# Kernel tuning notes

Hardware: AMD Instinct MI355X
Metric: run time of the kernel (lower is better)

Reference implementation:

```python
import jax, jax.numpy as jnp
import numpy as np

B, N, QDIM, KVDIM, DIM, H = 2, 4096, 256, 256, 256, 8


def setup_inputs() -> dict:
    key = jax.random.key(0)
    ks = jax.random.split(key, 8)
    s = 0.02
    return {
        "x": jax.random.normal(ks[0], (B, N, QDIM), jnp.float32),
        "y": jax.random.normal(ks[1], (B, N, KVDIM), jnp.float32),
        "Wq": jax.random.normal(ks[2], (DIM, QDIM), jnp.float32) * s,
        "bq": jnp.zeros((DIM,), jnp.float32),
        "Wk": jax.random.normal(ks[3], (DIM, KVDIM), jnp.float32) * s,
        "bk": jnp.zeros((DIM,), jnp.float32),
        "Wv": jax.random.normal(ks[4], (DIM, KVDIM), jnp.float32) * s,
        "bv": jnp.zeros((DIM,), jnp.float32),
        "Wo": jax.random.normal(ks[5], (DIM, DIM), jnp.float32) * s,
        "bo": jnp.zeros((DIM,), jnp.float32),
    }


def reference(x, y, Wq, bq, Wk, bk, Wv, bv, Wo, bo):
    b, n, _ = x.shape
    h = H
    scale = KVDIM ** (-0.5)  # note: full kv_dim, as in the source
    q = x @ Wq.T + bq  # (b, n, dim)
    k = y @ Wk.T + bk
    v = y @ Wv.T + bv
    def split(t):
        return t.reshape(b, -1, h, DIM // h).transpose(0, 2, 1, 3)  # b h n d
    q, k, v = split(q), split(k), split(v)
    dots = jnp.einsum('bhid,bhjd->bhij', q, k) * scale
    attn = jax.nn.softmax(dots, axis=-1)
    out = jnp.einsum('bhij,bhjd->bhid', attn, v)
    out = out.transpose(0, 2, 1, 3).reshape(b, n, DIM)  # b n (h d)
    out = out @ Wo.T + bo
    return out
```

## Files before the change

kernel.cpp:

```cpp
#include <hip/hip_runtime.h>

#define BATCH 2
#define SEQ   4096
#define DIM   256
#define NHEAD 8
#define HDIM  32
#define ROWS  (BATCH * SEQ)

typedef __attribute__((ext_vector_type(8))) short short8;
typedef __attribute__((ext_vector_type(8))) unsigned short ushort8;
typedef __attribute__((ext_vector_type(4))) unsigned short ushortx4;
typedef __attribute__((ext_vector_type(4))) float floatx4;
typedef __attribute__((ext_vector_type(2))) unsigned int uintx2;

static __device__ __forceinline__ unsigned short f2bf(float f) {
    union { float f; unsigned u; } v; v.f = f;
    unsigned r = v.u + 0x7fffu + ((v.u >> 16) & 1u);
    return (unsigned short)(r >> 16);
}
static __device__ __forceinline__ unsigned fbits(float f) {
    union { float f; unsigned u; } v; v.f = f; return v.u;
}
static __device__ __forceinline__ unsigned pack2(float a, float b) {
    return __builtin_amdgcn_perm(fbits(b), fbits(a), 0x07060302u);
}

static __device__ __forceinline__ void g2l16(const void* g, void* l) {
    __builtin_amdgcn_global_load_lds(
        (const __attribute__((address_space(1))) unsigned int*)g,
        (__attribute__((address_space(3))) unsigned int*)l, 16, 0, 0);
}

__global__ __launch_bounds__(256, 2) void qkv_kernel(
    const float* __restrict__ x, const float* __restrict__ y,
    const float* __restrict__ Wq, const float* __restrict__ Wk,
    const float* __restrict__ Wv,
    const float* __restrict__ bq, const float* __restrict__ bk, const float* __restrict__ bv,
    unsigned short* __restrict__ qo, unsigned short* __restrict__ ko,
    unsigned short* __restrict__ vto) {
    __shared__ unsigned short Abuf[8][64][32];
    const int tid = threadIdx.x, lane = tid & 63, wave = tid >> 6;
    const int ql = lane & 15, quad = lane >> 4;
    const int mat = blockIdx.y;
    const int m0 = blockIdx.x * 64;
    const float* A = (mat == 0) ? x : y;
    const float* W = (mat == 0) ? Wq : (mat == 1) ? Wk : Wv;
    const float* bias = (mat == 0) ? bq : (mat == 1) ? bk : bv;

    {
        const int row = tid >> 2, c8 = (tid & 3) * 8;
        const int swz = ((tid & 3) ^ ((row >> 1) & 3)) * 8;
        const float* src = A + (long)(m0 + row) * DIM + c8;
#pragma unroll
        for (int kb = 0; kb < 8; kb++) {
            float4 v0 = *(const float4*)(src + kb * 32);
            float4 v1 = *(const float4*)(src + kb * 32 + 4);
            ushort8 o;
            o[0] = f2bf(v0.x); o[1] = f2bf(v0.y); o[2] = f2bf(v0.z); o[3] = f2bf(v0.w);
            o[4] = f2bf(v1.x); o[5] = f2bf(v1.y); o[6] = f2bf(v1.z); o[7] = f2bf(v1.w);
            *(ushort8*)(&Abuf[kb][row][swz]) = o;
        }
    }
    __syncthreads();
    const int n0 = wave * 64;
    const int akey = (quad ^ ((ql >> 1) & 3)) * 8;
    floatx4 acc[4][4] = {};
    for (int kb = 0; kb < 8; kb++) {
        short8 wf[4], af[4];
#pragma unroll
        for (int u = 0; u < 4; u++) {
            const float* wr = W + (long)(n0 + u*16 + ql) * DIM + kb*32 + quad*8;
            float4 a = *(const float4*)wr;
            float4 c = *(const float4*)(wr + 4);
            short8 o;
            o[0] = (short)f2bf(a.x); o[1] = (short)f2bf(a.y); o[2] = (short)f2bf(a.z); o[3] = (short)f2bf(a.w);
            o[4] = (short)f2bf(c.x); o[5] = (short)f2bf(c.y); o[6] = (short)f2bf(c.z); o[7] = (short)f2bf(c.w);
            wf[u] = o;
        }
#pragma unroll
        for (int t = 0; t < 4; t++)
            af[t] = *(const short8*)(&Abuf[kb][t*16 + ql][akey]);
        if (mat < 2) {
#pragma unroll
            for (int t = 0; t < 4; t++)
#pragma unroll
                for (int u = 0; u < 4; u++)
                    acc[t][u] = __builtin_amdgcn_mfma_f32_16x16x32_bf16(wf[u], af[t], acc[t][u], 0, 0, 0);
        } else {
#pragma unroll
            for (int t = 0; t < 4; t++)
#pragma unroll
                for (int u = 0; u < 4; u++)
                    acc[t][u] = __builtin_amdgcn_mfma_f32_16x16x32_bf16(af[t], wf[u], acc[t][u], 0, 0, 0);
        }
    }
    if (mat < 2) {
        const float scale = (mat == 0) ? 0.09016844005556021f : 1.0f;
        unsigned short* out = (mat == 0) ? qo : ko;
#pragma unroll
        for (int t = 0; t < 4; t++) {
            int m = m0 + t*16 + ql;
#pragma unroll
            for (int u = 0; u < 4; u++) {
                int n = n0 + u*16 + quad*4;
                float4 b4 = *(const float4*)(bias + n);
                ushortx4 o;
                o.x = f2bf((acc[t][u][0] + b4.x) * scale);
                o.y = f2bf((acc[t][u][1] + b4.y) * scale);
                o.z = f2bf((acc[t][u][2] + b4.z) * scale);
                o.w = f2bf((acc[t][u][3] + b4.w) * scale);
                *(ushortx4*)(out + (long)m * DIM + n) = o;
            }
        }
    } else {
#pragma unroll
        for (int t = 0; t < 4; t++) {
            int mb = m0 + t*16 + quad*4;
            int bi = mb >> 12, i0 = mb & (SEQ - 1);
#pragma unroll
            for (int u = 0; u < 4; u++) {
                int n = n0 + u*16 + ql;
                float b = bias[n];
                ushortx4 o;
                o.x = f2bf(acc[t][u][0] + b);
                o.y = f2bf(acc[t][u][1] + b);
                o.z = f2bf(acc[t][u][2] + b);
                o.w = f2bf(acc[t][u][3] + b);
                *(ushortx4*)(vto + ((long)(bi * DIM + n)) * SEQ + i0) = o;
            }
        }
    }
}

__global__ __launch_bounds__(256, 2) void attn_kernel(
    const unsigned short* __restrict__ qb, const unsigned short* __restrict__ kbuf,
    const unsigned short* __restrict__ vT, unsigned short* __restrict__ ao) {
    __shared__ unsigned short K0[128 * 32], K1[128 * 32];
    __shared__ unsigned short V0[32 * 128], V1[32 * 128];
    __shared__ unsigned short P[4][32][72];
    const int tid = threadIdx.x, lane = tid & 63, wave = tid >> 6;
    const int ql = lane & 15, quad = lane >> 4;
    const int bh = blockIdx.y, b = bh >> 3, h = bh & 7;
    const int q0 = blockIdx.x * 128 + wave * 32;

    const unsigned short* qrow = qb   + (long)b * SEQ * DIM + h * HDIM;
    const unsigned short* krow = kbuf + (long)b * SEQ * DIM + h * HDIM;
    const unsigned short* vrow = vT   + (long)(b * DIM + h * HDIM) * SEQ;

    short8 qf[2];
#pragma unroll
    for (int t = 0; t < 2; t++)
        qf[t] = *(const short8*)(qrow + (long)(q0 + t*16 + ql) * DIM + quad*8);

    short8 ones;
#pragma unroll
    for (int i = 0; i < 8; i++) ones[i] = (short)0x3F80;

    const int kc0 = wave * 2, kc1 = wave * 2 + 1;
    const int klr = lane >> 2, kswz = ((lane & 3) ^ ((lane >> 3) & 3)) * 8;
    const unsigned short* kg0 = krow + (long)(kc0*16 + klr) * DIM + kswz;
    const unsigned short* kg1 = krow + (long)(kc1*16 + klr) * DIM + kswz;
    const int vlr = lane >> 4, vcl = lane & 15;
    const int vsw0 = (vcl ^ ((kc0*4 + vlr) & 7)) * 8;
    const int vsw1 = (vcl ^ ((kc1*4 + vlr) & 7)) * 8;
    const unsigned short* vg0 = vrow + (long)(kc0*4 + vlr) * SEQ + vsw0;
    const unsigned short* vg1 = vrow + (long)(kc1*4 + vlr) * SEQ + vsw1;

    const int kro = (quad ^ ((ql >> 1) & 3)) * 8;
    const int vmask = ql & 7;

    floatx4 acc[2][2] = {};
    floatx4 accL[2] = {};

    auto stage = [&](unsigned short* Kd, unsigned short* Vd, int kv0) {
        g2l16(kg0 + (long)kv0 * DIM, Kd + kc0 * 512);
        g2l16(kg1 + (long)kv0 * DIM, Kd + kc1 * 512);
        g2l16(vg0 + kv0, Vd + kc0 * 512);
        g2l16(vg1 + kv0, Vd + kc1 * 512);
    };
    auto compute = [&](const unsigned short* Ks, const unsigned short* Vs) {
#pragma unroll
        for (int half = 0; half < 2; ++half) {
#pragma unroll
            for (int mt = 0; mt < 4; ++mt) {
                short8 kf = *(const short8*)(Ks + (half*64 + mt*16 + ql) * 32 + kro);
#pragma unroll
                for (int t = 0; t < 2; t++) {
                    floatx4 z = {};
                    floatx4 s = __builtin_amdgcn_mfma_f32_16x16x32_bf16(kf, qf[t], z, 0, 0, 0);
                    float p0 = __builtin_amdgcn_exp2f(s[0]);
                    float p1 = __builtin_amdgcn_exp2f(s[1]);
                    float p2 = __builtin_amdgcn_exp2f(s[2]);
                    float p3 = __builtin_amdgcn_exp2f(s[3]);
                    uintx2 w;
                    w.x = pack2(p0, p1);
                    w.y = pack2(p2, p3);
                    *(uintx2*)(&P[wave][t*16 + ql][mt*16 + quad*4]) = w;
                }
            }
#pragma unroll
            for (int ks = 0; ks < 2; ++ks) {
                short8 pf[2];
#pragma unroll
                for (int t = 0; t < 2; t++)
                    pf[t] = *(const short8*)(&P[wave][t*16 + ql][ks*32 + quad*8]);
#pragma unroll
                for (int t = 0; t < 2; t++)
                    accL[t] = __builtin_amdgcn_mfma_f32_16x16x32_bf16(ones, pf[t], accL[t], 0, 0, 0);
#pragma unroll
                for (int dt = 0; dt < 2; ++dt) {
                    int vco = ((8*half + 4*ks + quad) ^ vmask) * 8;
                    short8 vf = *(const short8*)(Vs + (dt*16 + ql) * 128 + vco);
#pragma unroll
                    for (int t = 0; t < 2; t++)
                        acc[dt][t] = __builtin_amdgcn_mfma_f32_16x16x32_bf16(vf, pf[t], acc[dt][t], 0, 0, 0);
                }
            }
        }
    };

    stage(K0, V0, 0);
    __syncthreads();
    for (int it = 0; it < SEQ / 128; it += 2) {
        if (it + 1 < SEQ / 128) stage(K1, V1, (it + 1) * 128);
        compute(K0, V0);
        __syncthreads();
        if (it + 2 < SEQ / 128) stage(K0, V0, (it + 2) * 128);
        compute(K1, V1);
        __syncthreads();
    }

    float inv[2];
#pragma unroll
    for (int t = 0; t < 2; t++) inv[t] = 1.0f / accL[t][0];
#pragma unroll
    for (int dt = 0; dt < 2; dt++)
#pragma unroll
        for (int t = 0; t < 2; t++) {
            ushortx4 o;
            o.x = f2bf(acc[dt][t][0] * inv[t]);
            o.y = f2bf(acc[dt][t][1] * inv[t]);
            o.z = f2bf(acc[dt][t][2] * inv[t]);
            o.w = f2bf(acc[dt][t][3] * inv[t]);
            *(ushortx4*)(ao + (long)(b*SEQ + q0 + t*16 + ql) * DIM + h*HDIM + dt*16 + quad*4) = o;
        }
}

__global__ __launch_bounds__(256, 2) void oproj_kernel(
    const unsigned short* __restrict__ A, const float* __restrict__ W,
    const float* __restrict__ bias, float* __restrict__ out) {
    __shared__ unsigned short Abuf[8][32][32];
    const int tid = threadIdx.x, lane = tid & 63, wave = tid >> 6;
    const int ql = lane & 15, quad = lane >> 4;
    const int m0 = blockIdx.x * 32;
    const int swz = ((lane & 3) ^ ((lane >> 3) & 3)) * 8;
#pragma unroll
    for (int j = 0; j < 4; j++) {
        int c = wave * 4 + j;
        int kb = c >> 1, hf = (c & 1) * 16;
        const unsigned short* g = A + (long)(m0 + hf + (lane >> 2)) * DIM + kb*32 + swz;
        g2l16(g, &Abuf[kb][hf][0]);
    }
    __syncthreads();
    const int n0 = wave * 64;
    const int akey = (quad ^ ((ql >> 1) & 3)) * 8;
    floatx4 acc[2][4] = {};
    for (int kb = 0; kb < 8; kb++) {
        short8 wf[4], af[2];
#pragma unroll
        for (int u = 0; u < 4; u++) {
            const float* wr = W + (long)(n0 + u*16 + ql) * DIM + kb*32 + quad*8;
            float4 a = *(const float4*)wr;
            float4 c = *(const float4*)(wr + 4);
            short8 o;
            o[0] = (short)f2bf(a.x); o[1] = (short)f2bf(a.y); o[2] = (short)f2bf(a.z); o[3] = (short)f2bf(a.w);
            o[4] = (short)f2bf(c.x); o[5] = (short)f2bf(c.y); o[6] = (short)f2bf(c.z); o[7] = (short)f2bf(c.w);
            wf[u] = o;
        }
#pragma unroll
        for (int t = 0; t < 2; t++)
            af[t] = *(const short8*)(&Abuf[kb][t*16 + ql][akey]);
#pragma unroll
        for (int t = 0; t < 2; t++)
#pragma unroll
            for (int u = 0; u < 4; u++)
                acc[t][u] = __builtin_amdgcn_mfma_f32_16x16x32_bf16(wf[u], af[t], acc[t][u], 0, 0, 0);
    }
#pragma unroll
    for (int t = 0; t < 2; t++) {
        int m = m0 + t*16 + ql;
#pragma unroll
        for (int u = 0; u < 4; u++) {
            int n = n0 + u*16 + quad*4;
            float4 b4 = *(const float4*)(bias + n);
            float4 o;
            o.x = acc[t][u][0] + b4.x;
            o.y = acc[t][u][1] + b4.y;
            o.z = acc[t][u][2] + b4.z;
            o.w = acc[t][u][3] + b4.w;
            *(float4*)(out + (long)m * DIM + n) = o;
        }
    }
}

extern "C" void kernel_launch(void* const* d_in, const int* in_sizes, int n_in,
                              void* d_out, int out_size, void* d_ws, size_t ws_size,
                              hipStream_t stream) {
    const float* x  = (const float*)d_in[0];
    const float* y  = (const float*)d_in[1];
    const float* Wq = (const float*)d_in[2];
    const float* bq = (const float*)d_in[3];
    const float* Wk = (const float*)d_in[4];
    const float* bk = (const float*)d_in[5];
    const float* Wv = (const float*)d_in[6];
    const float* bv = (const float*)d_in[7];
    const float* Wo = (const float*)d_in[8];
    const float* bo = (const float*)d_in[9];
    float* out = (float*)d_out;

    const long NX = (long)ROWS * DIM;
    unsigned short* qbf  = (unsigned short*)d_ws;
    unsigned short* kbf  = qbf + NX;
    unsigned short* vTb  = kbf + NX;
    unsigned short* attn = vTb + NX;

    qkv_kernel<<<dim3(ROWS / 64, 3), dim3(256), 0, stream>>>(
        x, y, Wq, Wk, Wv, bq, bk, bv, qbf, kbf, vTb);

    attn_kernel<<<dim3(SEQ / 128, BATCH * NHEAD), dim3(256), 0, stream>>>(
        qbf, kbf, vTb, attn);

    oproj_kernel<<<dim3(ROWS / 32), dim3(256), 0, stream>>>(
        attn, Wo, bo, out);
}
```

Measured before the change: 169.9 us.

## Pre-convert inputs to bf16, retile projections, and enlarge attention query tile

Adds a separate conversion kernel that turns x, y and all weight matrices into bf16 once. The projection kernels can then stream A tiles with direct global-to-LDS loads, double-buffered, and read bf16 weights with no per-tile conversion. The QKV and output projections are retiled into 64x128 blocks with a 2x2 wave layout. Attention now handles 64 queries per wave with 64-key chunks and launch bounds of one block per SM. The cost is an extra kernel launch, extra memory traffic through the bf16 staging buffers, and a __syncthreads in every k-step; attention occupancy may also drop.

```diff
diff --git a/kernel.cpp b/kernel.cpp
--- a/kernel.cpp
+++ b/kernel.cpp
@@ -8,7 +8,6 @@
 #define ROWS  (BATCH * SEQ)
 
 typedef __attribute__((ext_vector_type(8))) short short8;
-typedef __attribute__((ext_vector_type(8))) unsigned short ushort8;
 typedef __attribute__((ext_vector_type(4))) unsigned short ushortx4;
 typedef __attribute__((ext_vector_type(4))) float floatx4;
 typedef __attribute__((ext_vector_type(2))) unsigned int uintx2;
@@ -24,85 +23,97 @@
 static __device__ __forceinline__ unsigned pack2(float a, float b) {
     return __builtin_amdgcn_perm(fbits(b), fbits(a), 0x07060302u);
 }
-
 static __device__ __forceinline__ void g2l16(const void* g, void* l) {
     __builtin_amdgcn_global_load_lds(
         (const __attribute__((address_space(1))) unsigned int*)g,
         (__attribute__((address_space(3))) unsigned int*)l, 16, 0, 0);
 }
 
-__global__ __launch_bounds__(256, 2) void qkv_kernel(
+__global__ __launch_bounds__(256) void convert_kernel(
     const float* __restrict__ x, const float* __restrict__ y,
     const float* __restrict__ Wq, const float* __restrict__ Wk,
-    const float* __restrict__ Wv,
+    const float* __restrict__ Wv, const float* __restrict__ Wo,
+    unsigned short* __restrict__ xb, unsigned short* __restrict__ yb,
+    unsigned short* __restrict__ Wqb, unsigned short* __restrict__ Wkb,
+    unsigned short* __restrict__ Wvb, unsigned short* __restrict__ Wob) {
+    const long NX = (long)ROWS * DIM;
+    const long NW = (long)DIM * DIM;
+    long e0 = ((long)blockIdx.x * 256 + threadIdx.x) * 4;
+    const float* src; unsigned short* dst; long off;
+    if      (e0 < NX)          { src = x;  dst = xb;  off = e0; }
+    else if (e0 < 2*NX)        { src = y;  dst = yb;  off = e0 - NX; }
+    else if (e0 < 2*NX + NW)   { src = Wq; dst = Wqb; off = e0 - 2*NX; }
+    else if (e0 < 2*NX + 2*NW) { src = Wk; dst = Wkb; off = e0 - 2*NX - NW; }
+    else if (e0 < 2*NX + 3*NW) { src = Wv; dst = Wvb; off = e0 - 2*NX - 2*NW; }
+    else if (e0 < 2*NX + 4*NW) { src = Wo; dst = Wob; off = e0 - 2*NX - 3*NW; }
+    else return;
+    float4 v = *(const float4*)(src + off);
+    ushortx4 o;
+    o.x = f2bf(v.x); o.y = f2bf(v.y); o.z = f2bf(v.z); o.w = f2bf(v.w);
+    *(ushortx4*)(dst + off) = o;
+}
+
+__global__ __launch_bounds__(256, 2) void qkv_kernel(
+    const unsigned short* __restrict__ xb, const unsigned short* __restrict__ yb,
+    const unsigned short* __restrict__ Wq, const unsigned short* __restrict__ Wk,
+    const unsigned short* __restrict__ Wv,
     const float* __restrict__ bq, const float* __restrict__ bk, const float* __restrict__ bv,
     unsigned short* __restrict__ qo, unsigned short* __restrict__ ko,
     unsigned short* __restrict__ vto) {
-    __shared__ unsigned short Abuf[8][64][32];
+    __shared__ unsigned short Ab0[64 * 32], Ab1[64 * 32];
     const int tid = threadIdx.x, lane = tid & 63, wave = tid >> 6;
     const int ql = lane & 15, quad = lane >> 4;
-    const int mat = blockIdx.y;
+    const int wm = wave & 1, wn = wave >> 1;
+    const int mat = blockIdx.z;
     const int m0 = blockIdx.x * 64;
-    const float* A = (mat == 0) ? x : y;
-    const float* W = (mat == 0) ? Wq : (mat == 1) ? Wk : Wv;
+    const int n0 = blockIdx.y * 128;
+    const unsigned short* A = (mat == 0) ? xb : yb;
+    const unsigned short* W = (mat == 0) ? Wq : (mat == 1) ? Wk : Wv;
     const float* bias = (mat == 0) ? bq : (mat == 1) ? bk : bv;
 
-    {
-        const int row = tid >> 2, c8 = (tid & 3) * 8;
-        const int swz = ((tid & 3) ^ ((row >> 1) & 3)) * 8;
-        const float* src = A + (long)(m0 + row) * DIM + c8;
-#pragma unroll
-        for (int kb = 0; kb < 8; kb++) {
-            float4 v0 = *(const float4*)(src + kb * 32);
-            float4 v1 = *(const float4*)(src + kb * 32 + 4);
-            ushort8 o;
-            o[0] = f2bf(v0.x); o[1] = f2bf(v0.y); o[2] = f2bf(v0.z); o[3] = f2bf(v0.w);
-            o[4] = f2bf(v1.x); o[5] = f2bf(v1.y); o[6] = f2bf(v1.z); o[7] = f2bf(v1.w);
-            *(ushort8*)(&Abuf[kb][row][swz]) = o;
-        }
-    }
+    const unsigned short* ag = A + (long)(m0 + wave*16 + (lane >> 2)) * DIM
+                                 + ((lane & 3) ^ ((lane >> 3) & 3)) * 8;
+    unsigned short* ad0 = Ab0 + wave * 512;
+    unsigned short* ad1 = Ab1 + wave * 512;
+    const int akey = (quad ^ ((ql >> 1) & 3)) * 8;
+
+    floatx4 acc[2][4] = {};
+    g2l16(ag, ad0);
     __syncthreads();
-    const int n0 = wave * 64;
-    const int akey = (quad ^ ((ql >> 1) & 3)) * 8;
-    floatx4 acc[4][4] = {};
     for (int kb = 0; kb < 8; kb++) {
-        short8 wf[4], af[4];
-#pragma unroll
-        for (int u = 0; u < 4; u++) {
-            const float* wr = W + (long)(n0 + u*16 + ql) * DIM + kb*32 + quad*8;
-            float4 a = *(const float4*)wr;
-            float4 c = *(const float4*)(wr + 4);
-            short8 o;
-            o[0] = (short)f2bf(a.x); o[1] = (short)f2bf(a.y); o[2] = (short)f2bf(a.z); o[3] = (short)f2bf(a.w);
-            o[4] = (short)f2bf(c.x); o[5] = (short)f2bf(c.y); o[6] = (short)f2bf(c.z); o[7] = (short)f2bf(c.w);
-            wf[u] = o;
-        }
-#pragma unroll
-        for (int t = 0; t < 4; t++)
-            af[t] = *(const short8*)(&Abuf[kb][t*16 + ql][akey]);
+        if (kb < 7) g2l16(ag + (kb + 1) * 32, (kb & 1) ? ad0 : ad1);
+        const unsigned short* Ას = (kb & 1) ? Ab1 : Ab0;
+        short8 wf[4], af[2];
+#pragma unroll
+        for (int u = 0; u < 4; u++)
+            wf[u] = *(const short8*)(W + (long)(n0 + wn*64 + u*16 + ql) * DIM + kb*32 + quad*8);
+#pragma unroll
+        for (int t = 0; t < 2; t++)
+            af[t] = *(const short8*)(Ას + (wm*32 + t*16 + ql) * 32 + akey);
         if (mat < 2) {
 #pragma unroll
-            for (int t = 0; t < 4; t++)
+            for (int t = 0; t < 2; t++)
 #pragma unroll
                 for (int u = 0; u < 4; u++)
                     acc[t][u] = __builtin_amdgcn_mfma_f32_16x16x32_bf16(wf[u], af[t], acc[t][u], 0, 0, 0);
         } else {
 #pragma unroll
-            for (int t = 0; t < 4; t++)
+            for (int t = 0; t < 2; t++)
 #pragma unroll
                 for (int u = 0; u < 4; u++)
                     acc[t][u] = __builtin_amdgcn_mfma_f32_16x16x32_bf16(af[t], wf[u], acc[t][u], 0, 0, 0);
         }
+        __syncthreads();
     }
     if (mat < 2) {
         const float scale = (mat == 0) ? 0.09016844005556021f : 1.0f;
         unsigned short* out = (mat == 0) ? qo : ko;
 #pragma unroll
-        for (int t = 0; t < 4; t++) {
-            int m = m0 + t*16 + ql;
+        for (int t = 0; t < 2; t++) {
+            int m = m0 + wm*32 + t*16 + ql;
 #pragma unroll
             for (int u = 0; u < 4; u++) {
-                int n = n0 + u*16 + quad*4;
+                int n = n0 + wn*64 + u*16 + quad*4;
                 float4 b4 = *(const float4*)(bias + n);
                 ushortx4 o;
                 o.x = f2bf((acc[t][u][0] + b4.x) * scale);
@@ -114,12 +125,12 @@
         }
     } else {
 #pragma unroll
-        for (int t = 0; t < 4; t++) {
-            int mb = m0 + t*16 + quad*4;
+        for (int t = 0; t < 2; t++) {
+            int mb = m0 + wm*32 + t*16 + quad*4;
             int bi = mb >> 12, i0 = mb & (SEQ - 1);
 #pragma unroll
             for (int u = 0; u < 4; u++) {
-                int n = n0 + u*16 + ql;
+                int n = n0 + wn*64 + u*16 + ql;
                 float b = bias[n];
                 ushortx4 o;
                 o.x = f2bf(acc[t][u][0] + b);
@@ -132,111 +143,103 @@
     }
 }
 
-__global__ __launch_bounds__(256, 2) void attn_kernel(
+__global__ __launch_bounds__(256, 1) void attn_kernel(
     const unsigned short* __restrict__ qb, const unsigned short* __restrict__ kbuf,
     const unsigned short* __restrict__ vT, unsigned short* __restrict__ ao) {
-    __shared__ unsigned short K0[128 * 32], K1[128 * 32];
-    __shared__ unsigned short V0[32 * 128], V1[32 * 128];
-    __shared__ unsigned short P[4][32][72];
+    __shared__ unsigned short K0[64 * 32], K1[64 * 32];
+    __shared__ unsigned short V0[32 * 64], V1[32 * 64];
+    __shared__ unsigned short P[4][64][72];
     const int tid = threadIdx.x, lane = tid & 63, wave = tid >> 6;
     const int ql = lane & 15, quad = lane >> 4;
     const int bh = blockIdx.y, b = bh >> 3, h = bh & 7;
-    const int q0 = blockIdx.x * 128 + wave * 32;
+    const int q0 = blockIdx.x * 256 + wave * 64;
 
     const unsigned short* qrow = qb   + (long)b * SEQ * DIM + h * HDIM;
     const unsigned short* krow = kbuf + (long)b * SEQ * DIM + h * HDIM;
     const unsigned short* vrow = vT   + (long)(b * DIM + h * HDIM) * SEQ;
 
-    short8 qf[2];
-#pragma unroll
-    for (int t = 0; t < 2; t++)
+    short8 qf[4];
+#pragma unroll
+    for (int t = 0; t < 4; t++)
         qf[t] = *(const short8*)(qrow + (long)(q0 + t*16 + ql) * DIM + quad*8);
 
     short8 ones;
 #pragma unroll
     for (int i = 0; i < 8; i++) ones[i] = (short)0x3F80;
 
-    const int kc0 = wave * 2, kc1 = wave * 2 + 1;
-    const int klr = lane >> 2, kswz = ((lane & 3) ^ ((lane >> 3) & 3)) * 8;
-    const unsigned short* kg0 = krow + (long)(kc0*16 + klr) * DIM + kswz;
-    const unsigned short* kg1 = krow + (long)(kc1*16 + klr) * DIM + kswz;
-    const int vlr = lane >> 4, vcl = lane & 15;
-    const int vsw0 = (vcl ^ ((kc0*4 + vlr) & 7)) * 8;
-    const int vsw1 = (vcl ^ ((kc1*4 + vlr) & 7)) * 8;
-    const unsigned short* vg0 = vrow + (long)(kc0*4 + vlr) * SEQ + vsw0;
-    const unsigned short* vg1 = vrow + (long)(kc1*4 + vlr) * SEQ + vsw1;
-
+    const unsigned short* kg = krow + (long)(wave*16 + (lane >> 2)) * DIM
+                                    + ((lane & 3) ^ ((lane >> 3) & 3)) * 8;
+    const unsigned short* vg = vrow + (long)(wave*8 + (lane >> 3)) * SEQ
+                                    + ((lane & 7) ^ (lane >> 3)) * 8;
+    unsigned short* kd0 = K0 + wave * 512;  unsigned short* kd1 = K1 + wave * 512;
+    unsigned short* vd0 = V0 + wave * 512;  unsigned short* vd1 = V1 + wave * 512;
     const int kro = (quad ^ ((ql >> 1) & 3)) * 8;
     const int vmask = ql & 7;
 
-    floatx4 acc[2][2] = {};
-    floatx4 accL[2] = {};
-
-    auto stage = [&](unsigned short* Kd, unsigned short* Vd, int kv0) {
-        g2l16(kg0 + (long)kv0 * DIM, Kd + kc0 * 512);
-        g2l16(kg1 + (long)kv0 * DIM, Kd + kc1 * 512);
-        g2l16(vg0 + kv0, Vd + kc0 * 512);
-        g2l16(vg1 + kv0, Vd + kc1 * 512);
+    floatx4 acc[2][4] = {};
+    floatx4 accL[4] = {};
+
+    auto compute = [&](const unsigned short* Ks, const unsigned short* Vs) {
+#pragma unroll
+        for (int mt = 0; mt < 4; ++mt) {
+            short8 kf = *(const short8*)(Ks + (mt*16 + ql) * 32 + kro);
+#pragma unroll
+            for (int t = 0; t < 4; t++) {
+                floatx4 z = {};
+                floatx4 s = __builtin_amdgcn_mfma_f32_16x16x32_bf16(kf, qf[t], z, 0, 0, 0);
+                float p0 = __builtin_amdgcn_exp2f(s[0]);
+                float p1 = __builtin_amdgcn_exp2f(s[1]);
+                float p2 = __builtin_amdgcn_exp2f(s[2]);
+                float p3 = __builtin_amdgcn_exp2f(s[3]);
+                uintx2 w;
+                w.x = pack2(p0, p1);
+                w.y = pack2(p2, p3);
+                *(uintx2*)(&P[wave][t*16 + ql][mt*16 + quad*4]) = w;
+            }
+        }
+#pragma unroll
+        for (int ks = 0; ks < 2; ++ks) {
+            short8 pf[4];
+#pragma unroll
+            for (int t = 0; t < 4; t++)
+                pf[t] = *(const short8*)(&P[wave][t*16 + ql][ks*32 + quad*8]);
+#pragma unroll
+            for (int t = 0; t < 4; t++)
+                accL[t] = __builtin_amdgcn_mfma_f32_16x16x32_bf16(ones, pf[t], accL[t], 0, 0, 0);
+#pragma unroll
+            for (int dt = 0; dt < 2; ++dt) {
+                short8 vf = *(const short8*)(Vs + (dt*16 + ql) * 64 + ((ks*4 + quad) ^ vmask) * 8);
+#pragma unroll
+                for (int t = 0; t < 4; t++)
+                    acc[dt][t] = __builtin_amdgcn_mfma_f32_16x16x32_bf16(vf, pf[t], acc[dt][t], 0, 0, 0);
+            }
+        }
     };
-    auto compute = [&](const unsigned short* Ks, const unsigned short* Vs) {
-#pragma unroll
-        for (int half = 0; half < 2; ++half) {
-#pragma unroll
-            for (int mt = 0; mt < 4; ++mt) {
-                short8 kf = *(const short8*)(Ks + (half*64 + mt*16 + ql) * 32 + kro);
-#pragma unroll
-                for (int t = 0; t < 2; t++) {
-                    floatx4 z = {};
-                    floatx4 s = __builtin_amdgcn_mfma_f32_16x16x32_bf16(kf, qf[t], z, 0, 0, 0);
-                    float p0 = __builtin_amdgcn_exp2f(s[0]);
-                    float p1 = __builtin_amdgcn_exp2f(s[1]);
-                    float p2 = __builtin_amdgcn_exp2f(s[2]);
-                    float p3 = __builtin_amdgcn_exp2f(s[3]);
-                    uintx2 w;
-                    w.x = pack2(p0, p1);
-                    w.y = pack2(p2, p3);
-                    *(uintx2*)(&P[wave][t*16 + ql][mt*16 + quad*4]) = w;
-                }
-            }
-#pragma unroll
-            for (int ks = 0; ks < 2; ++ks) {
-                short8 pf[2];
-#pragma unroll
-                for (int t = 0; t < 2; t++)
-                    pf[t] = *(const short8*)(&P[wave][t*16 + ql][ks*32 + quad*8]);
-#pragma unroll
-                for (int t = 0; t < 2; t++)
-                    accL[t] = __builtin_amdgcn_mfma_f32_16x16x32_bf16(ones, pf[t], accL[t], 0, 0, 0);
-#pragma unroll
-                for (int dt = 0; dt < 2; ++dt) {
-                    int vco = ((8*half + 4*ks + quad) ^ vmask) * 8;
-                    short8 vf = *(const short8*)(Vs + (dt*16 + ql) * 128 + vco);
-#pragma unroll
-                    for (int t = 0; t < 2; t++)
-                        acc[dt][t] = __builtin_amdgcn_mfma_f32_16x16x32_bf16(vf, pf[t], acc[dt][t], 0, 0, 0);
-                }
-            }
-        }
-    };
-
-    stage(K0, V0, 0);
+
+    g2l16(kg, kd0); g2l16(vg, vd0);
     __syncthreads();
-    for (int it = 0; it < SEQ / 128; it += 2) {
-        if (it + 1 < SEQ / 128) stage(K1, V1, (it + 1) * 128);
+    for (int it = 0; it < SEQ / 64; it += 2) {
+        if (it + 1 < SEQ / 64) {
+            g2l16(kg + (long)(it + 1) * 64 * DIM, kd1);
+            g2l16(vg + (it + 1) * 64, vd1);
+        }
         compute(K0, V0);
         __syncthreads();
-        if (it + 2 < SEQ / 128) stage(K0, V0, (it + 2) * 128);
+        if (it + 2 < SEQ / 64) {
+            g2l16(kg + (long)(it + 2) * 64 * DIM, kd0);
+            g2l16(vg + (it + 2) * 64, vd0);
+        }
         compute(K1, V1);
         __syncthreads();
     }
 
-    float inv[2];
-#pragma unroll
-    for (int t = 0; t < 2; t++) inv[t] = 1.0f / accL[t][0];
+    float inv[4];
+#pragma unroll
+    for (int t = 0; t < 4; t++) inv[t] = 1.0f / accL[t][0];
 #pragma unroll
     for (int dt = 0; dt < 2; dt++)
 #pragma unroll
-        for (int t = 0; t < 2; t++) {
+        for (int t = 0; t < 4; t++) {
             ushortx4 o;
             o.x = f2bf(acc[dt][t][0] * inv[t]);
             o.y = f2bf(acc[dt][t][1] * inv[t]);
@@ -247,51 +250,47 @@
 }
 
 __global__ __launch_bounds__(256, 2) void oproj_kernel(
-    const unsigned short* __restrict__ A, const float* __restrict__ W,
+    const unsigned short* __restrict__ A, const unsigned short* __restrict__ W,
     const float* __restrict__ bias, float* __restrict__ out) {
-    __shared__ unsigned short Abuf[8][32][32];
+    __shared__ unsigned short Ab0[64 * 32], Ab1[64 * 32];
     const int tid = threadIdx.x, lane = tid & 63, wave = tid >> 6;
     const int ql = lane & 15, quad = lane >> 4;
-    const int m0 = blockIdx.x * 32;
-    const int swz = ((lane & 3) ^ ((lane >> 3) & 3)) * 8;
-#pragma unroll
-    for (int j = 0; j < 4; j++) {
-        int c = wave * 4 + j;
-        int kb = c >> 1, hf = (c & 1) * 16;
-        const unsigned short* g = A + (long)(m0 + hf + (lane >> 2)) * DIM + kb*32 + swz;
-        g2l16(g, &Abuf[kb][hf][0]);
-    }
+    const int wm = wave & 1, wn = wave >> 1;
+    const int m0 = blockIdx.x * 64;
+    const int n0 = blockIdx.y * 128;
+
+    const unsigned short* ag = A + (long)(m0 + wave*16 + (lane >> 2)) * DIM
+                                 + ((lane & 3) ^ ((lane >> 3) & 3)) * 8;
+    unsigned short* ad0 = Ab0 + wave * 512;
+    unsigned short* ad1 = Ab1 + wave * 512;
+    const int akey = (quad ^ ((ql >> 1) & 3)) * 8;
+
+    floatx4 acc[2][4] = {};
+    g2l16(ag, ad0);
     __syncthreads();
-    const int n0 = wave * 64;
-    const int akey = (quad ^ ((ql >> 1) & 3)) * 8;
-    floatx4 acc[2][4] = {};
     for (int kb = 0; kb < 8; kb++) {
+        if (kb < 7) g2l16(ag + (kb + 1) * 32, (kb & 1) ? ad0 : ad1);
+        const unsigned short* As = (kb & 1) ? Ab1 : Ab0;
         short8 wf[4], af[2];
 #pragma unroll
-        for (int u = 0; u < 4; u++) {
-            const float* wr = W + (long)(n0 + u*16 + ql) * DIM + kb*32 + quad*8;
-            float4 a = *(const float4*)wr;
-            float4 c = *(const float4*)(wr + 4);
-            short8 o;
-            o[0] = (short)f2bf(a.x); o[1] = (short)f2bf(a.y); o[2] = (short)f2bf(a.z); o[3] = (short)f2bf(a.w);
-            o[4] = (short)f2bf(c.x); o[5] = (short)f2bf(c.y); o[6] = (short)f2bf(c.z); o[7] = (short)f2bf(c.w);
-            wf[u] = o;
-        }
+        for (int u = 0; u < 4; u++)
+            wf[u] = *(const short8*)(W + (long)(n0 + wn*64 + u*16 + ql) * DIM + kb*32 + quad*8);
 #pragma unroll
         for (int t = 0; t < 2; t++)
-            af[t] = *(const short8*)(&Abuf[kb][t*16 + ql][akey]);
+            af[t] = *(const short8*)(As + (wm*32 + t*16 + ql) * 32 + akey);
 #pragma unroll
         for (int t = 0; t < 2; t++)
 #pragma unroll
             for (int u = 0; u < 4; u++)
                 acc[t][u] = __builtin_amdgcn_mfma_f32_16x16x32_bf16(wf[u], af[t], acc[t][u], 0, 0, 0);
+        __syncthreads();
     }
 #pragma unroll
     for (int t = 0; t < 2; t++) {
-        int m = m0 + t*16 + ql;
+        int m = m0 + wm*32 + t*16 + ql;
 #pragma unroll
         for (int u = 0; u < 4; u++) {
-            int n = n0 + u*16 + quad*4;
+            int n = n0 + wn*64 + u*16 + quad*4;
             float4 b4 = *(const float4*)(bias + n);
             float4 o;
             o.x = acc[t][u][0] + b4.x;
@@ -319,17 +318,28 @@
     float* out = (float*)d_out;
 
     const long NX = (long)ROWS * DIM;
-    unsigned short* qbf  = (unsigned short*)d_ws;
+    const long NW = (long)DIM * DIM;
+    unsigned short* xb   = (unsigned short*)d_ws;
+    unsigned short* yb   = xb  + NX;
+    unsigned short* Wqb  = yb  + NX;
+    unsigned short* Wkb  = Wqb + NW;
+    unsigned short* Wvb  = Wkb + NW;
+    unsigned short* Wob  = Wvb + NW;
+    unsigned short* qbf  = Wob + NW;
     unsigned short* kbf  = qbf + NX;
     unsigned short* vTb  = kbf + NX;
     unsigned short* attn = vTb + NX;
 
-    qkv_kernel<<<dim3(ROWS / 64, 3), dim3(256), 0, stream>>>(
-        x, y, Wq, Wk, Wv, bq, bk, bv, qbf, kbf, vTb);
-
-    attn_kernel<<<dim3(SEQ / 128, BATCH * NHEAD), dim3(256), 0, stream>>>(
+    long total4 = (2*NX + 4*NW) / 4;
+    convert_kernel<<<dim3((unsigned)((total4 + 255) / 256)), dim3(256), 0, stream>>>(
+        x, y, Wq, Wk, Wv, Wo, xb, yb, Wqb, Wkb, Wvb, Wob);
+
+    qkv_kernel<<<dim3(ROWS / 64, 2, 3), dim3(256), 0, stream>>>(
+        xb, yb, Wqb, Wkb, Wvb, bq, bk, bv, qbf, kbf, vTb);
+
+    attn_kernel<<<dim3(SEQ / 256, BATCH * NHEAD), dim3(256), 0, stream>>>(
         qbf, kbf, vTb, attn);
 
-    oproj_kernel<<<dim3(ROWS / 32), dim3(256), 0, stream>>>(
-        attn, Wo, bo, out);
-}
+    oproj_kernel<<<dim3(ROWS / 64, 2), dim3(256), 0, stream>>>(
+        attn, Wob, bo, out);
+}
```

New measurement: 190.2 us. 1.12x slower.
